# Kernel tuning notes

Measured on AMD Instinct MI355X. Metric: run time of the kernel, lower is better.

Reference implementation:

```python
import jax, jax.numpy as jnp
import numpy as np

B = 4096
INPUT_SIZE = 1000
HIDDEN = 512
NUM_MASKS = 4
GROUP_SIZE = 100  # int(1000 * 0.1)
NUM_GROUPS = INPUT_SIZE // GROUP_SIZE  # 10, divides evenly


def entmax(alpha, v):
    # matches the torch helper: softmax-like with alpha-power denominator
    v = v - jnp.max(v, axis=-1, keepdims=True)
    e = jnp.exp(v)
    s = (jnp.sum(e ** alpha, axis=-1, keepdims=True) + 1e-5) ** (1.0 / alpha)
    return e / s


def layernorm(h, w, b):
    # h: [..., H]; w,b broadcast to [..., H]
    mu = jnp.mean(h, axis=-1, keepdims=True)
    var = jnp.mean((h - mu) ** 2, axis=-1, keepdims=True)
    return (h - mu) * jax.lax.rsqrt(var + 1e-5) * w + b


def setup_inputs() -> dict:
    key = jax.random.key(0)
    ks = jax.random.split(key, 4)
    x = jax.random.normal(ks[0], (B, INPUT_SIZE), dtype=jnp.float32)
    W_masks = jax.random.normal(ks[1], (NUM_GROUPS, NUM_MASKS, GROUP_SIZE), dtype=jnp.float32)
    W1 = jax.random.normal(ks[2], (NUM_GROUPS, HIDDEN, GROUP_SIZE), dtype=jnp.float32)
    W2 = jax.random.normal(ks[3], (NUM_GROUPS, HIDDEN, GROUP_SIZE), dtype=jnp.float32)
    ln1_w = jnp.ones((NUM_GROUPS, HIDDEN), dtype=jnp.float32)
    ln1_b = jnp.zeros((NUM_GROUPS, HIDDEN), dtype=jnp.float32)
    ln2_w = jnp.ones((NUM_GROUPS, HIDDEN), dtype=jnp.float32)
    ln2_b = jnp.zeros((NUM_GROUPS, HIDDEN), dtype=jnp.float32)
    return {"x": x, "W_masks": W_masks, "W1": W1, "W2": W2,
            "ln1_w": ln1_w, "ln1_b": ln1_b, "ln2_w": ln2_w, "ln2_b": ln2_b}


def reference(x, W_masks, W1, W2, ln1_w, ln1_b, ln2_w, ln2_b):
    G, M, S = W_masks.shape
    b = x.shape[0]
    xg = x.reshape(b, G, S)                                  # [B,G,S]
    mask = entmax(1.1, W_masks)                              # [G,M,S]
    weighted = xg[:, :, None, :] * mask[None]                # [B,G,M,S]
    h1 = jnp.einsum('bgms,ghs->bgmh', weighted, W1)          # [B,G,M,H]
    h2 = jnp.einsum('bgms,ghs->bgmh', weighted, W2)
    n1 = layernorm(h1, ln1_w[None, :, None, :], ln1_b[None, :, None, :])
    n2 = layernorm(h2, ln2_w[None, :, None, :], ln2_b[None, :, None, :])
    activated = jax.nn.relu(jax.nn.sigmoid(n1) * n2)         # [B,G,M,H]
    group_out = jnp.sum(activated, axis=2)                   # [B,G,H]
    return group_out.reshape(b, G * group_out.shape[-1])     # [B, G*H]
```

## Files before the change

kernel.cpp:

```cpp
#include <hip/hip_runtime.h>
#include <math.h>

typedef _Float16 half8 __attribute__((ext_vector_type(8)));
typedef float f32x4 __attribute__((ext_vector_type(4)));

namespace {
constexpr int BATCH = 4096;
constexpr int IN  = 1000;
constexpr int G   = 10;
constexpr int M   = 4;
constexpr int S   = 100;
constexpr int H   = 512;
constexpr int BB  = 16;
constexpr int R   = 64;
constexpr int NT  = 512;
constexpr int KP  = 128;
constexpr int WXP = 136;
constexpr int OFF_XS  = R * WXP * 2;
constexpr int OFF_MSK = OFF_XS + BB * S * 4;
constexpr int LDS_SZ  = OFF_MSK + M * S * 4;
constexpr int OFF_FIN = 64 * 9 * 16;
constexpr size_t WMAT = (size_t)G * H * KP;
constexpr size_t W16_BYTES = 2 * WMAT * sizeof(_Float16);
}

__global__ __launch_bounds__(256)
void cvt_w_kernel(const float* __restrict__ W1, const float* __restrict__ W2,
                  _Float16* __restrict__ w16) {
  const int t = blockIdx.x * 256 + threadIdx.x;
  const int c = t & 15;
  const int row = t >> 4;
  const int mat = row / (G * H);
  const int r2  = row - mat * (G * H);
  const float* src = (mat ? W2 : W1) + (size_t)r2 * S;
  union { _Float16 h[8]; uint4 u; } o;
  #pragma unroll
  for (int j = 0; j < 8; ++j) {
    const int k = c * 8 + j;
    o.h[j] = (k < S) ? (_Float16)src[k] : (_Float16)0.f;
  }
  *(uint4*)&w16[(size_t)row * KP + c * 8] = o.u;
}

__device__ inline half8 pk8(float4 a, float4 b) {
  half8 r;
  r[0] = (_Float16)a.x; r[1] = (_Float16)a.y; r[2] = (_Float16)a.z; r[3] = (_Float16)a.w;
  r[4] = (_Float16)b.x; r[5] = (_Float16)b.y; r[6] = (_Float16)b.z; r[7] = (_Float16)b.w;
  return r;
}

template <bool PRE>
__global__ __launch_bounds__(NT, 2)
void dfg_mfma3_kernel(const float* __restrict__ x,
                      const float* __restrict__ Wm,
                      const _Float16* __restrict__ w16,
                      const float* __restrict__ W1f,
                      const float* __restrict__ W2f,
                      const float* __restrict__ ln1w,
                      const float* __restrict__ ln1b,
                      const float* __restrict__ ln2w,
                      const float* __restrict__ ln2b,
                      float* __restrict__ out) {
  __shared__ __align__(16) char smem[LDS_SZ];
  _Float16* wxs = (_Float16*)smem;
  float*    xs  = (float*)(smem + OFF_XS);
  float*    msk = (float*)(smem + OFF_MSK);
  float4*   red = (float4*)smem;
  float4*   fin = (float4*)(smem + OFF_FIN);

  const int tid = threadIdx.x;
  const int id      = blockIdx.x;
  const int logical = (id & 7) * 320 + (id >> 3);
  const int g  = logical >> 8;
  const int b0 = (logical & 255) * BB;

  const int wv = tid >> 6, l = tid & 63;
  const int lo = l & 15, hi = l >> 4;

  for (int f = tid; f < BB * 25; f += NT) {
    int bl = f / 25, s4 = f - bl * 25;
    *(float4*)&xs[bl * S + s4 * 4] =
        *(const float4*)(x + (size_t)(b0 + bl) * IN + g * S + s4 * 4);
  }
  if (wv < 4) {
    const float* wmp = Wm + (g * M + wv) * S;
    float v0 = (l < S) ? wmp[l] : -INFINITY;
    float v1 = (l + 64 < S) ? wmp[l + 64] : -INFINITY;
    float mx = fmaxf(v0, v1);
    #pragma unroll
    for (int d = 32; d >= 1; d >>= 1) mx = fmaxf(mx, __shfl_xor(mx, d));
    float e0 = (l < S) ? expf(v0 - mx) : 0.f;
    float e1 = (l + 64 < S) ? expf(v1 - mx) : 0.f;
    float a0 = (l < S) ? expf(1.1f * (v0 - mx)) : 0.f;
    float a1 = (l + 64 < S) ? expf(1.1f * (v1 - mx)) : 0.f;
    float ss = a0 + a1;
    #pragma unroll
    for (int d = 32; d >= 1; d >>= 1) ss += __shfl_xor(ss, d);
    float inv = 1.0f / powf(ss + 1e-5f, 1.0f / 1.1f);
    if (l < S) msk[wv * S + l] = e0 * inv;
    if (l + 64 < S) msk[wv * S + l + 64] = e1 * inv;
  }
  __syncthreads();

  {
    const int r = tid >> 3;
    const int j = tid & 7;
    const int bl = r & 15, m = r >> 4;
    union { _Float16 h[16]; uint4 u[2]; } o;
    #pragma unroll
    for (int i = 0; i < 16; ++i) {
      const int k = j * 16 + i;
      float v = 0.f;
      if (k < S) v = xs[bl * S + k] * msk[m * S + k];
      o.h[i] = (_Float16)v;
    }
    *(uint4*)&wxs[r * WXP + j * 16]     = o.u[0];
    *(uint4*)&wxs[r * WXP + j * 16 + 8] = o.u[1];
  }
  __syncthreads();

  f32x4 acc1[4][4] = {};
  f32x4 acc2[4][4] = {};
  const _Float16* w1p = PRE ? w16 + (size_t)g * H * KP : nullptr;
  const _Float16* w2p = PRE ? w1p + WMAT : nullptr;
  const float* W1g = W1f + (size_t)g * H * S;
  const float* W2g = W2f + (size_t)g * H * S;

  #pragma unroll
  for (int ks = 0; ks < 4; ++ks) {
    half8 xf[4];
    #pragma unroll
    for (int rt = 0; rt < 4; ++rt)
      xf[rt] = *(const half8*)&wxs[(rt * 16 + lo) * WXP + ks * 32 + 8 * hi];
    #pragma unroll
    for (int ht = 0; ht < 4; ++ht) {
      const int hrow = 64 * wv + ht * 16 + lo;
      half8 wf1, wf2;
      if constexpr (PRE) {
        wf1 = *(const half8*)&w1p[(size_t)hrow * KP + ks * 32 + 8 * hi];
        wf2 = *(const half8*)&w2p[(size_t)hrow * KP + ks * 32 + 8 * hi];
      } else {
        const float* s1 = W1g + (size_t)hrow * S + ks * 32 + 8 * hi;
        const float* s2 = W2g + (size_t)hrow * S + ks * 32 + 8 * hi;
        if (ks < 3) {
          wf1 = pk8(*(const float4*)s1, *(const float4*)(s1 + 4));
          wf2 = pk8(*(const float4*)s2, *(const float4*)(s2 + 4));
        } else if (hi == 0) {
          float4 z = make_float4(0.f, 0.f, 0.f, 0.f);
          wf1 = pk8(*(const float4*)s1, z);
          wf2 = pk8(*(const float4*)s2, z);
        } else {
          half8 zz = {};
          wf1 = zz; wf2 = zz;
        }
      }
      #pragma unroll
      for (int rt = 0; rt < 4; ++rt) {
        acc1[ht][rt] = __builtin_amdgcn_mfma_f32_16x16x32_f16(wf1, xf[rt], acc1[ht][rt], 0, 0, 0);
        acc2[ht][rt] = __builtin_amdgcn_mfma_f32_16x16x32_f16(wf2, xf[rt], acc2[ht][rt], 0, 0, 0);
      }
    }
  }
  __syncthreads();

  float st1[4], sq1[4], st2[4], sq2[4];
  #pragma unroll
  for (int rt = 0; rt < 4; ++rt) {
    float s1 = 0.f, q1 = 0.f, s2 = 0.f, q2 = 0.f;
    #pragma unroll
    for (int ht = 0; ht < 4; ++ht)
      #pragma unroll
      for (int rg = 0; rg < 4; ++rg) {
        float a = acc1[ht][rt][rg], b = acc2[ht][rt][rg];
        s1 += a; q1 += a * a; s2 += b; q2 += b * b;
      }
    st1[rt] = s1; sq1[rt] = q1; st2[rt] = s2; sq2[rt] = q2;
  }
  #pragma unroll
  for (int d = 16; d <= 32; d <<= 1) {
    #pragma unroll
    for (int rt = 0; rt < 4; ++rt) {
      st1[rt] += __shfl_xor(st1[rt], d); sq1[rt] += __shfl_xor(sq1[rt], d);
      st2[rt] += __shfl_xor(st2[rt], d); sq2[rt] += __shfl_xor(sq2[rt], d);
    }
  }
  if (hi == 0) {
    #pragma unroll
    for (int rt = 0; rt < 4; ++rt)
      red[(rt * 16 + lo) * 9 + wv] = make_float4(st1[rt], sq1[rt], st2[rt], sq2[rt]);
  }
  __syncthreads();
  if (tid < 64) {
    float4 t = make_float4(0.f, 0.f, 0.f, 0.f);
    #pragma unroll
    for (int j = 0; j < 8; ++j) {
      float4 v = red[tid * 9 + j];
      t.x += v.x; t.y += v.y; t.z += v.z; t.w += v.w;
    }
    float mu1 = t.x * (1.f / H), mu2 = t.z * (1.f / H);
    float va = t.y * (1.f / H) - mu1 * mu1;
    float vb = t.w * (1.f / H) - mu2 * mu2;
    fin[tid] = make_float4(mu1, rsqrtf(va + 1e-5f), mu2, rsqrtf(vb + 1e-5f));
  }
  __syncthreads();

  float4 fr[4];
  #pragma unroll
  for (int rt = 0; rt < 4; ++rt) fr[rt] = fin[rt * 16 + lo];
  const float* p1w = ln1w + g * H; const float* p1b = ln1b + g * H;
  const float* p2w = ln2w + g * H; const float* p2b = ln2b + g * H;
  float* orow = out + (size_t)(b0 + lo) * (G * H) + g * H;
  #pragma unroll
  for (int ht = 0; ht < 4; ++ht) {
    const int hb = 64 * wv + ht * 16 + 4 * hi;
    float4 w1v = *(const float4*)(p1w + hb);
    float4 b1v = *(const float4*)(p1b + hb);
    float4 w2v = *(const float4*)(p2w + hb);
    float4 b2v = *(const float4*)(p2b + hb);
    float o[4] = {0.f, 0.f, 0.f, 0.f};
    #pragma unroll
    for (int rt = 0; rt < 4; ++rt) {
      #pragma unroll
      for (int rg = 0; rg < 4; ++rg) {
        float n1 = (acc1[ht][rt][rg] - fr[rt].x) * fr[rt].y * (&w1v.x)[rg] + (&b1v.x)[rg];
        float n2 = (acc2[ht][rt][rg] - fr[rt].z) * fr[rt].w * (&w2v.x)[rg] + (&b2v.x)[rg];
        float sg = 1.0f / (1.0f + __expf(-n1));
        o[rg] += fmaxf(sg * n2, 0.f);
      }
    }
    *(float4*)(orow + hb) = make_float4(o[0], o[1], o[2], o[3]);
  }
}

extern "C" void kernel_launch(void* const* d_in, const int* in_sizes, int n_in,
                              void* d_out, int out_size, void* d_ws, size_t ws_size,
                              hipStream_t stream) {
  const float* x   = (const float*)d_in[0];
  const float* Wm  = (const float*)d_in[1];
  const float* W1  = (const float*)d_in[2];
  const float* W2  = (const float*)d_in[3];
  const float* l1w = (const float*)d_in[4];
  const float* l1b = (const float*)d_in[5];
  const float* l2w = (const float*)d_in[6];
  const float* l2b = (const float*)d_in[7];
  float* outp = (float*)d_out;

  const dim3 grid((BATCH / BB) * G);
  if (ws_size >= W16_BYTES && d_ws != nullptr) {
    _Float16* w16 = (_Float16*)d_ws;
    const int cvt_threads = 2 * G * H * (KP / 8);
    cvt_w_kernel<<<cvt_threads / 256, 256, 0, stream>>>(W1, W2, w16);
    dfg_mfma3_kernel<true><<<grid, NT, 0, stream>>>(
        x, Wm, w16, W1, W2, l1w, l1b, l2w, l2b, outp);
  } else {
    dfg_mfma3_kernel<false><<<grid, NT, 0, stream>>>(
        x, Wm, nullptr, W1, W2, l1w, l1b, l2w, l2b, outp);
  }
}
```

Before: 285.5 us.

## Register double-buffer fp16 weight fragments and relax launch bounds

In the precomputed-weight path, the weight fragments for the next K step are loaded from global memory into registers while the MFMAs for the current step run. The goal is to hide global load latency behind MFMA work. Launch bounds drop from 2 to 1 blocks per SM, so the compiler can use more registers for the extra buffers, at the cost of lower occupancy. The sigmoid divide is also replaced with a hardware reciprocal approximation.

```diff
diff --git a/kernel.cpp b/kernel.cpp
--- a/kernel.cpp
+++ b/kernel.cpp
@@ -50,8 +50,8 @@
 }
 
 template <bool PRE>
-__global__ __launch_bounds__(NT, 2)
-void dfg_mfma3_kernel(const float* __restrict__ x,
+__global__ __launch_bounds__(NT, 1)
+void dfg_mfma4_kernel(const float* __restrict__ x,
                       const float* __restrict__ Wm,
                       const _Float16* __restrict__ w16,
                       const float* __restrict__ W1f,
@@ -126,20 +126,54 @@
   const float* W1g = W1f + (size_t)g * H * S;
   const float* W2g = W2f + (size_t)g * H * S;
 
-  #pragma unroll
-  for (int ks = 0; ks < 4; ++ks) {
-    half8 xf[4];
-    #pragma unroll
-    for (int rt = 0; rt < 4; ++rt)
-      xf[rt] = *(const half8*)&wxs[(rt * 16 + lo) * WXP + ks * 32 + 8 * hi];
+  if constexpr (PRE) {
+    half8 cw1[4], cw2[4];
     #pragma unroll
     for (int ht = 0; ht < 4; ++ht) {
-      const int hrow = 64 * wv + ht * 16 + lo;
-      half8 wf1, wf2;
-      if constexpr (PRE) {
-        wf1 = *(const half8*)&w1p[(size_t)hrow * KP + ks * 32 + 8 * hi];
-        wf2 = *(const half8*)&w2p[(size_t)hrow * KP + ks * 32 + 8 * hi];
-      } else {
+      const size_t off = (size_t)(64 * wv + ht * 16 + lo) * KP + 8 * hi;
+      cw1[ht] = *(const half8*)&w1p[off];
+      cw2[ht] = *(const half8*)&w2p[off];
+    }
+    #pragma unroll
+    for (int ks = 0; ks < 4; ++ks) {
+      half8 nw1[4], nw2[4];
+      if (ks < 3) {
+        #pragma unroll
+        for (int ht = 0; ht < 4; ++ht) {
+          const size_t off =
+              (size_t)(64 * wv + ht * 16 + lo) * KP + (ks + 1) * 32 + 8 * hi;
+          nw1[ht] = *(const half8*)&w1p[off];
+          nw2[ht] = *(const half8*)&w2p[off];
+        }
+      }
+      half8 xf[4];
+      #pragma unroll
+      for (int rt = 0; rt < 4; ++rt)
+        xf[rt] = *(const half8*)&wxs[(rt * 16 + lo) * WXP + ks * 32 + 8 * hi];
+      #pragma unroll
+      for (int ht = 0; ht < 4; ++ht) {
+        #pragma unroll
+        for (int rt = 0; rt < 4; ++rt) {
+          acc1[ht][rt] = __builtin_amdgcn_mfma_f32_16x16x32_f16(cw1[ht], xf[rt], acc1[ht][rt], 0, 0, 0);
+          acc2[ht][rt] = __builtin_amdgcn_mfma_f32_16x16x32_f16(cw2[ht], xf[rt], acc2[ht][rt], 0, 0, 0);
+        }
+      }
+      if (ks < 3) {
+        #pragma unroll
+        for (int ht = 0; ht < 4; ++ht) { cw1[ht] = nw1[ht]; cw2[ht] = nw2[ht]; }
+      }
+    }
+  } else {
+    #pragma unroll
+    for (int ks = 0; ks < 4; ++ks) {
+      half8 xf[4];
+      #pragma unroll
+      for (int rt = 0; rt < 4; ++rt)
+        xf[rt] = *(const half8*)&wxs[(rt * 16 + lo) * WXP + ks * 32 + 8 * hi];
+      #pragma unroll
+      for (int ht = 0; ht < 4; ++ht) {
+        const int hrow = 64 * wv + ht * 16 + lo;
+        half8 wf1, wf2;
         const float* s1 = W1g + (size_t)hrow * S + ks * 32 + 8 * hi;
         const float* s2 = W2g + (size_t)hrow * S + ks * 32 + 8 * hi;
         if (ks < 3) {
@@ -153,11 +187,11 @@
           half8 zz = {};
           wf1 = zz; wf2 = zz;
         }
-      }
-      #pragma unroll
-      for (int rt = 0; rt < 4; ++rt) {
-        acc1[ht][rt] = __builtin_amdgcn_mfma_f32_16x16x32_f16(wf1, xf[rt], acc1[ht][rt], 0, 0, 0);
-        acc2[ht][rt] = __builtin_amdgcn_mfma_f32_16x16x32_f16(wf2, xf[rt], acc2[ht][rt], 0, 0, 0);
+        #pragma unroll
+        for (int rt = 0; rt < 4; ++rt) {
+          acc1[ht][rt] = __builtin_amdgcn_mfma_f32_16x16x32_f16(wf1, xf[rt], acc1[ht][rt], 0, 0, 0);
+          acc2[ht][rt] = __builtin_amdgcn_mfma_f32_16x16x32_f16(wf2, xf[rt], acc2[ht][rt], 0, 0, 0);
+        }
       }
     }
   }
@@ -224,7 +258,7 @@
       for (int rg = 0; rg < 4; ++rg) {
         float n1 = (acc1[ht][rt][rg] - fr[rt].x) * fr[rt].y * (&w1v.x)[rg] + (&b1v.x)[rg];
         float n2 = (acc2[ht][rt][rg] - fr[rt].z) * fr[rt].w * (&w2v.x)[rg] + (&b2v.x)[rg];
-        float sg = 1.0f / (1.0f + __expf(-n1));
+        float sg = __builtin_amdgcn_rcpf(1.0f + __expf(-n1));
         o[rg] += fmaxf(sg * n2, 0.f);
       }
     }
@@ -250,10 +284,10 @@
     _Float16* w16 = (_Float16*)d_ws;
     const int cvt_threads = 2 * G * H * (KP / 8);
     cvt_w_kernel<<<cvt_threads / 256, 256, 0, stream>>>(W1, W2, w16);
-    dfg_mfma3_kernel<true><<<grid, NT, 0, stream>>>(
+    dfg_mfma4_kernel<true><<<grid, NT, 0, stream>>>(
         x, Wm, w16, W1, W2, l1w, l1b, l2w, l2b, outp);
   } else {
-    dfg_mfma3_kernel<false><<<grid, NT, 0, stream>>>(
+    dfg_mfma4_kernel<false><<<grid, NT, 0, stream>>>(
         x, Wm, nullptr, W1, W2, l1w, l1b, l2w, l2b, outp);
   }
 }
```

Result: faster. 265.8 us (-6.9%).
